# Kernel optimization log

Hardware: AMD Instinct MI355X
Metric: run time of the kernel (lower is better)

The kernel has to match this reference:

```python
import jax, jax.numpy as jnp
import numpy as np

IN_DIM = 256
QK_DIM = IN_DIM // 8  # 32
B, H, W = 4, 64, 64


def setup_inputs() -> dict:
    key = jax.random.key(0)
    ks = jax.random.split(key, 8)
    s = 1.0 / np.sqrt(IN_DIM)
    return {
        "x": jax.random.normal(ks[0], (B, IN_DIM, H, W), dtype=jnp.float32),
        "Wq": jax.random.normal(ks[1], (QK_DIM, IN_DIM), dtype=jnp.float32) * s,
        "bq": jax.random.normal(ks[2], (QK_DIM,), dtype=jnp.float32) * 0.01,
        "Wk": jax.random.normal(ks[3], (QK_DIM, IN_DIM), dtype=jnp.float32) * s,
        "bk": jax.random.normal(ks[4], (QK_DIM,), dtype=jnp.float32) * 0.01,
        "Wv": jax.random.normal(ks[5], (IN_DIM, IN_DIM), dtype=jnp.float32) * s,
        "bv": jax.random.normal(ks[6], (IN_DIM,), dtype=jnp.float32) * 0.01,
        "gamma": jax.random.normal(ks[7], (1,), dtype=jnp.float32) * 0.1,
    }


def reference(x, Wq, bq, Wk, bk, Wv, bv, gamma):
    b, c, h, w = x.shape
    n = h * w
    xf = x.reshape(b, c, n)  # [b, c, n]
    # 1x1 convs are channel-wise linear maps over flattened spatial dim
    q = jnp.einsum('dc,bcn->bnd', Wq, xf) + bq  # [b, n, d]
    k = jnp.einsum('dc,bcn->bdn', Wk, xf) + bk[:, None]  # [b, d, n]
    attn = jax.nn.softmax(jnp.einsum('bnd,bdm->bnm', q, k), axis=-1)  # [b, n, n]
    v = jnp.einsum('ec,bcn->ben', Wv, xf) + bv[:, None]  # [b, c, n]
    # out[:, :, m] = sum_n v[:, :, n] * attn[m, n]  (bmm with attn^T)
    out = jnp.einsum('ben,bmn->bem', v, attn).reshape(b, c, h, w)
    return gamma * out + x
```

## Files before the change

### kernel.cpp

```cpp
#include <hip/hip_runtime.h>
#include <hip/hip_bf16.h>
#include <stdint.h>

#define DI __device__ __forceinline__

typedef float f32x4 __attribute__((ext_vector_type(4)));
typedef short bf16x8 __attribute__((ext_vector_type(8)));

constexpr int BATCH = 4;
constexpr int C = 256;
constexpr int N = 4096;
constexpr int NO = 320;
constexpr int KB2 = 64;
constexpr int NT2 = N / KB2;
constexpr float LOG2E = 1.44269504088896340736f;

DI unsigned short f2bf(float f) {
  union { float f; unsigned int i; } v; v.f = f;
  unsigned int r = v.i + 0x7fffu + ((v.i >> 16) & 1u);
  return (unsigned short)(r >> 16);
}

DI float exp2i(float x) {
  float r; asm("v_exp_f32 %0, %1" : "=v"(r) : "v"(x)); return r;
}

DI unsigned int cvtpk(float lo, float hi) {
  unsigned int r;
  asm("v_cvt_pk_bf16_f32 %0, %1, %2" : "=v"(r) : "v"(lo), "v"(hi));
  return r;
}

__global__ __launch_bounds__(256) void prep_kernel(
    const float* __restrict__ Wq, const float* __restrict__ Wk, const float* __restrict__ Wv,
    const float* __restrict__ bq, const float* __restrict__ bk, const float* __restrict__ bv,
    unsigned short* __restrict__ Wcat, float* __restrict__ bcat) {
  int idx = blockIdx.x * 256 + threadIdx.x;
  if (idx < NO * C) {
    int row = idx >> 8, c = idx & 255;
    float v = (row < 32) ? Wq[row * 256 + c] * LOG2E
            : (row < 64) ? Wk[(row - 32) * 256 + c]
                         : Wv[(row - 64) * 256 + c];
    Wcat[idx] = f2bf(v);
  }
  if (idx < NO) {
    float v = (idx < 32) ? bq[idx] * LOG2E
            : (idx < 64) ? bk[idx - 32] : bv[idx - 64];
    bcat[idx] = v;
  }
}

__global__ __launch_bounds__(256) void proj_kernel(
    const float* __restrict__ x, const unsigned short* __restrict__ Wcat,
    const float* __restrict__ bcat,
    unsigned short* __restrict__ qarr, unsigned short* __restrict__ karr,
    unsigned short* __restrict__ vT) {
  __shared__ __align__(16) unsigned short ldsx[C][66];

  int b = blockIdx.y, n0 = blockIdx.x * 64, z = blockIdx.z;
  int t = threadIdx.x, lane = t & 63, w = t >> 6;
  int g = lane >> 4, cq = lane & 15;

  const float* xb = x + (size_t)b * C * N;
  {
    int csub = lane >> 4, m = lane & 15;
    #pragma unroll 4
    for (int cc = 0; cc < 16; ++cc) {
      int c = cc * 16 + w * 4 + csub;
      f32x4 v = *(const f32x4*)(xb + (size_t)c * N + n0 + m * 4);
      unsigned int p01 = ((unsigned int)f2bf(v[0])) | ((unsigned int)f2bf(v[1]) << 16);
      unsigned int p23 = ((unsigned int)f2bf(v[2])) | ((unsigned int)f2bf(v[3]) << 16);
      *(unsigned int*)(&ldsx[c][m * 4]) = p01;
      *(unsigned int*)(&ldsx[c][m * 4 + 2]) = p23;
    }
  }
  __syncthreads();

  bf16x8 afrag[8];
  int nrow = w * 16 + cq;
  #pragma unroll
  for (int ks = 0; ks < 8; ++ks) {
    bf16x8 a;
    #pragma unroll
    for (int j = 0; j < 8; ++j) a[j] = (short)ldsx[ks * 32 + g * 8 + j][nrow];
    afrag[ks] = a;
  }
  __syncthreads();

  unsigned short (*vlds)[66] = (unsigned short (*)[66]) & ldsx[0][0];

  #pragma unroll
  for (int i = 0; i < 4; ++i) {
    int oc = z * 4 + i;
    int o = oc * 16 + cq;
    f32x4 acc = {0.f, 0.f, 0.f, 0.f};
    const unsigned short* wrow = Wcat + o * 256;
    #pragma unroll
    for (int ks = 0; ks < 8; ++ks) {
      bf16x8 bf = *(const bf16x8*)(wrow + ks * 32 + g * 8);
      acc = __builtin_amdgcn_mfma_f32_16x16x32_bf16(afrag[ks], bf, acc, 0, 0, 0);
    }
    float bias = bcat[o];
    if (z == 0) {
      unsigned short* dst = (oc < 2) ? qarr : karr;
      int od = ((oc & 1) << 4) + cq;
      #pragma unroll
      for (int r = 0; r < 4; ++r) {
        int n = n0 + w * 16 + g * 4 + r;
        dst[((size_t)b * N + n) * 32 + od] = f2bf(acc[r] + bias);
      }
    } else {
      int el = i * 16 + cq;
      #pragma unroll
      for (int r = 0; r < 4; ++r)
        vlds[w * 16 + g * 4 + r][el] = f2bf(acc[r] + bias);
    }
  }

  if (z > 0) {
    __syncthreads();
    int e0 = (z - 1) * 64;
    #pragma unroll 4
    for (int ep = 0; ep < 16; ++ep) {
      int el = ep * 4 + w;
      vT[((size_t)b * 256 + e0 + el) * N + n0 + lane] = vlds[lane][el];
    }
  }
}

__global__ __launch_bounds__(512) void attn_kernel(
    const unsigned short* __restrict__ qarr, const unsigned short* __restrict__ karr,
    const unsigned short* __restrict__ vT, const float* __restrict__ x,
    const float* __restrict__ gamma_p, float* __restrict__ out) {
  __shared__ __align__(16) unsigned int plds[2][64][36];
  __shared__ float lsc[64];

  int bid = blockIdx.x;
  int xcd = bid & 7;
  int b = xcd >> 1;
  int eh = (bid >> 3) & 1;
  int tile = ((bid >> 4) << 1) | (bid & 1);

  int t = threadIdx.x, lane = t & 63, w = t >> 6;
  int g = lane >> 4, cq = lane & 15;
  int qw = w & 3, kh = w >> 2;

  const unsigned short* kb = karr + (size_t)b * N * 32;
  const unsigned short* vTb = vT + (size_t)b * C * N;

  bf16x8 qf = *(const bf16x8*)(qarr + ((size_t)b * N + tile * 64 + qw * 16 + cq) * 32 + g * 8);

  short onev = (cq == 0) ? (short)0x3F80 : (short)0;
  bf16x8 onesA = {onev, onev, onev, onev, onev, onev, onev, onev};

  f32x4 o[4];
  #pragma unroll
  for (int j = 0; j < 4; ++j) o[j] = f32x4{0.f, 0.f, 0.f, 0.f};
  f32x4 oL = {0.f, 0.f, 0.f, 0.f};

  const unsigned short* vbase = vTb + (size_t)(eh * 128 + w * 16 + cq) * N + g * 8;
  const unsigned short* kbase0 = kb + (size_t)(kh * 32 + 2 * cq) * 32 + g * 8;

  bf16x8 kf0 = *(const bf16x8*)(kbase0);
  bf16x8 kf1 = *(const bf16x8*)(kbase0 + 32);
  bf16x8 vf0 = *(const bf16x8*)(vbase);
  bf16x8 vf1 = *(const bf16x8*)(vbase + 32);

  const float C2 = 20.0f * LOG2E;

  for (int nt = 0; nt < NT2; ++nt) {
    int pb = nt & 1;
    int nn2 = ((nt + 1) & (NT2 - 1)) * KB2;

    bf16x8 nk0 = *(const bf16x8*)(kbase0 + (size_t)nn2 * 32);
    bf16x8 nk1 = *(const bf16x8*)(kbase0 + (size_t)nn2 * 32 + 32);
    bf16x8 nv0 = *(const bf16x8*)(vbase + nn2);
    bf16x8 nv1 = *(const bf16x8*)(vbase + nn2 + 32);

    f32x4 s0 = __builtin_amdgcn_mfma_f32_16x16x32_bf16(qf, kf0, f32x4{0.f,0.f,0.f,0.f}, 0, 0, 0);
    f32x4 s1 = __builtin_amdgcn_mfma_f32_16x16x32_bf16(qf, kf1, f32x4{0.f,0.f,0.f,0.f}, 0, 0, 0);

    #pragma unroll
    for (int r = 0; r < 4; ++r) {
      float p0 = exp2i(s0[r] - C2);
      float p1 = exp2i(s1[r] - C2);
      plds[pb][qw * 16 + g * 4 + r][kh * 16 + cq] = cvtpk(p0, p1);
    }

    asm volatile("s_waitcnt lgkmcnt(0)\n\ts_barrier" ::: "memory");

    __builtin_amdgcn_s_setprio(1);
    #pragma unroll
    for (int qc = 0; qc < 4; ++qc) {
      const unsigned short* prow = (const unsigned short*)&plds[pb][qc * 16 + cq][0];
      bf16x8 pf0 = *(const bf16x8*)(prow + g * 8);
      bf16x8 pf1 = *(const bf16x8*)(prow + 32 + g * 8);
      o[qc] = __builtin_amdgcn_mfma_f32_16x16x32_bf16(vf0, pf0, o[qc], 0, 0, 0);
      o[qc] = __builtin_amdgcn_mfma_f32_16x16x32_bf16(vf1, pf1, o[qc], 0, 0, 0);
      if (qc == w) {
        oL = __builtin_amdgcn_mfma_f32_16x16x32_bf16(onesA, pf0, oL, 0, 0, 0);
        oL = __builtin_amdgcn_mfma_f32_16x16x32_bf16(onesA, pf1, oL, 0, 0, 0);
      }
    }
    __builtin_amdgcn_s_setprio(0);

    kf0 = nk0; kf1 = nk1; vf0 = nv0; vf1 = nv1;
  }

  if (w < 4 && lane < 16) lsc[w * 16 + lane] = gamma_p[0] / oL[0];
  __syncthreads();

  const float* xb = x + (size_t)b * C * N;
  float* ob = out + (size_t)b * C * N;
  #pragma unroll
  for (int qc = 0; qc < 4; ++qc) {
    float scale = lsc[qc * 16 + cq];
    int qg = tile * 64 + qc * 16 + cq;
    #pragma unroll
    for (int r = 0; r < 4; ++r) {
      int e = eh * 128 + w * 16 + g * 4 + r;
      size_t idx = (size_t)e * N + qg;
      ob[idx] = o[qc][r] * scale + xb[idx];
    }
  }
}

extern "C" void kernel_launch(void* const* d_in, const int* in_sizes, int n_in,
                              void* d_out, int out_size, void* d_ws, size_t ws_size,
                              hipStream_t stream) {
  const float* x  = (const float*)d_in[0];
  const float* Wq = (const float*)d_in[1];
  const float* bq = (const float*)d_in[2];
  const float* Wk = (const float*)d_in[3];
  const float* bk = (const float*)d_in[4];
  const float* Wv = (const float*)d_in[5];
  const float* bv = (const float*)d_in[6];
  const float* gamma = (const float*)d_in[7];
  float* out = (float*)d_out;

  char* ws = (char*)d_ws;
  unsigned short* Wcat = (unsigned short*)(ws);
  float* bcat          = (float*)(ws + 163840);
  unsigned short* qarr = (unsigned short*)(ws + 165120);
  unsigned short* karr = (unsigned short*)(ws + 1213696);
  unsigned short* vT   = (unsigned short*)(ws + 2262272);

  prep_kernel<<<320, 256, 0, stream>>>(Wq, Wk, Wv, bq, bk, bv, Wcat, bcat);
  proj_kernel<<<dim3(64, 4, 5), 256, 0, stream>>>(x, Wcat, bcat, qarr, karr, vT);
  attn_kernel<<<512, 512, 0, stream>>>(qarr, karr, vT, x, gamma, out);
}
```

Measured before the change: 225.5 us.

## Retile attention to 32 queries by all channels and split projection grid finer

The attention kernel now gives each block 32 queries across all 256 output channels instead of 64 queries across half the channels. This removes the duplicated QK^T and exp work that the two channel-half blocks used to repeat, and it replaces the ones-matrix MFMA row-sum with per-lane fp32 accumulation followed by shuffle and LDS reduction. In exchange, each block streams the full V tile, which doubles total V reads from L2, and each wave holds more V fragments. Separately, the projection kernel's output split is doubled to 10 z-slices to increase parallelism, at the cost of reloading x into LDS more often.

New measurement: 241.0 us. 1.07x slower.

```diff
diff --git a/kernel.cpp b/kernel.cpp
--- a/kernel.cpp
+++ b/kernel.cpp
@@ -23,12 +23,6 @@
 
 DI float exp2i(float x) {
   float r; asm("v_exp_f32 %0, %1" : "=v"(r) : "v"(x)); return r;
-}
-
-DI unsigned int cvtpk(float lo, float hi) {
-  unsigned int r;
-  asm("v_cvt_pk_bf16_f32 %0, %1, %2" : "=v"(r) : "v"(lo), "v"(hi));
-  return r;
 }
 
 __global__ __launch_bounds__(256) void prep_kernel(
@@ -90,8 +84,8 @@
   unsigned short (*vlds)[66] = (unsigned short (*)[66]) & ldsx[0][0];
 
   #pragma unroll
-  for (int i = 0; i < 4; ++i) {
-    int oc = z * 4 + i;
+  for (int i = 0; i < 2; ++i) {
+    int oc = z * 2 + i;
     int o = oc * 16 + cq;
     f32x4 acc = {0.f, 0.f, 0.f, 0.f};
     const unsigned short* wrow = Wcat + o * 256;
@@ -101,8 +95,8 @@
       acc = __builtin_amdgcn_mfma_f32_16x16x32_bf16(afrag[ks], bf, acc, 0, 0, 0);
     }
     float bias = bcat[o];
-    if (z == 0) {
-      unsigned short* dst = (oc < 2) ? qarr : karr;
+    if (z < 2) {
+      unsigned short* dst = (z == 0) ? qarr : karr;
       int od = ((oc & 1) << 4) + cq;
       #pragma unroll
       for (int r = 0; r < 4; ++r) {
@@ -117,54 +111,56 @@
     }
   }
 
-  if (z > 0) {
+  if (z >= 2) {
     __syncthreads();
-    int e0 = (z - 1) * 64;
+    int e0 = (z - 2) * 32;
     #pragma unroll 4
-    for (int ep = 0; ep < 16; ++ep) {
+    for (int ep = 0; ep < 8; ++ep) {
       int el = ep * 4 + w;
       vT[((size_t)b * 256 + e0 + el) * N + n0 + lane] = vlds[lane][el];
     }
   }
 }
 
-__global__ __launch_bounds__(512) void attn_kernel(
+__global__ __launch_bounds__(512, 4) void attn_kernel(
     const unsigned short* __restrict__ qarr, const unsigned short* __restrict__ karr,
     const unsigned short* __restrict__ vT, const float* __restrict__ x,
     const float* __restrict__ gamma_p, float* __restrict__ out) {
-  __shared__ __align__(16) unsigned int plds[2][64][36];
-  __shared__ float lsc[64];
+  __shared__ __align__(16) unsigned short plds[2][32][136];
+  __shared__ float lred[4][32];
+  __shared__ float lsc[32];
 
   int bid = blockIdx.x;
   int xcd = bid & 7;
   int b = xcd >> 1;
-  int eh = (bid >> 3) & 1;
-  int tile = ((bid >> 4) << 1) | (bid & 1);
+  int tile = ((bid >> 3) << 1) | (bid & 1);
 
   int t = threadIdx.x, lane = t & 63, w = t >> 6;
   int g = lane >> 4, cq = lane & 15;
-  int qw = w & 3, kh = w >> 2;
+  int qw = w & 1, kh = w >> 1;
 
   const unsigned short* kb = karr + (size_t)b * N * 32;
   const unsigned short* vTb = vT + (size_t)b * C * N;
 
-  bf16x8 qf = *(const bf16x8*)(qarr + ((size_t)b * N + tile * 64 + qw * 16 + cq) * 32 + g * 8);
-
-  short onev = (cq == 0) ? (short)0x3F80 : (short)0;
-  bf16x8 onesA = {onev, onev, onev, onev, onev, onev, onev, onev};
-
-  f32x4 o[4];
-  #pragma unroll
-  for (int j = 0; j < 4; ++j) o[j] = f32x4{0.f, 0.f, 0.f, 0.f};
-  f32x4 oL = {0.f, 0.f, 0.f, 0.f};
-
-  const unsigned short* vbase = vTb + (size_t)(eh * 128 + w * 16 + cq) * N + g * 8;
-  const unsigned short* kbase0 = kb + (size_t)(kh * 32 + 2 * cq) * 32 + g * 8;
-
-  bf16x8 kf0 = *(const bf16x8*)(kbase0);
-  bf16x8 kf1 = *(const bf16x8*)(kbase0 + 32);
-  bf16x8 vf0 = *(const bf16x8*)(vbase);
-  bf16x8 vf1 = *(const bf16x8*)(vbase + 32);
+  bf16x8 qf = *(const bf16x8*)(qarr + ((size_t)b * N + tile * 32 + qw * 16 + cq) * 32 + g * 8);
+
+  f32x4 o[2][2];
+  #pragma unroll
+  for (int i = 0; i < 2; ++i)
+    #pragma unroll
+    for (int j = 0; j < 2; ++j) o[i][j] = f32x4{0.f, 0.f, 0.f, 0.f};
+  float Ls[4] = {0.f, 0.f, 0.f, 0.f};
+
+  const unsigned short* vbase = vTb + (size_t)(w * 32 + cq) * N + g * 8;
+  const unsigned short* kbase = kb + (size_t)(kh * 16 + cq) * 32 + g * 8;
+
+  bf16x8 kf = *(const bf16x8*)(kbase);
+  bf16x8 vf[2][2];
+  #pragma unroll
+  for (int ec = 0; ec < 2; ++ec)
+    #pragma unroll
+    for (int kc = 0; kc < 2; ++kc)
+      vf[ec][kc] = *(const bf16x8*)(vbase + (size_t)ec * 16 * N + kc * 32);
 
   const float C2 = 20.0f * LOG2E;
 
@@ -172,55 +168,76 @@
     int pb = nt & 1;
     int nn2 = ((nt + 1) & (NT2 - 1)) * KB2;
 
-    bf16x8 nk0 = *(const bf16x8*)(kbase0 + (size_t)nn2 * 32);
-    bf16x8 nk1 = *(const bf16x8*)(kbase0 + (size_t)nn2 * 32 + 32);
-    bf16x8 nv0 = *(const bf16x8*)(vbase + nn2);
-    bf16x8 nv1 = *(const bf16x8*)(vbase + nn2 + 32);
-
-    f32x4 s0 = __builtin_amdgcn_mfma_f32_16x16x32_bf16(qf, kf0, f32x4{0.f,0.f,0.f,0.f}, 0, 0, 0);
-    f32x4 s1 = __builtin_amdgcn_mfma_f32_16x16x32_bf16(qf, kf1, f32x4{0.f,0.f,0.f,0.f}, 0, 0, 0);
+    bf16x8 nk = *(const bf16x8*)(kbase + (size_t)nn2 * 32);
+    bf16x8 nv[2][2];
+    #pragma unroll
+    for (int ec = 0; ec < 2; ++ec)
+      #pragma unroll
+      for (int kc = 0; kc < 2; ++kc)
+        nv[ec][kc] = *(const bf16x8*)(vbase + (size_t)ec * 16 * N + nn2 + kc * 32);
+
+    f32x4 s = __builtin_amdgcn_mfma_f32_16x16x32_bf16(qf, kf, f32x4{0.f,0.f,0.f,0.f}, 0, 0, 0);
 
     #pragma unroll
     for (int r = 0; r < 4; ++r) {
-      float p0 = exp2i(s0[r] - C2);
-      float p1 = exp2i(s1[r] - C2);
-      plds[pb][qw * 16 + g * 4 + r][kh * 16 + cq] = cvtpk(p0, p1);
+      float p = exp2i(s[r] - C2);
+      Ls[r] += p;
+      plds[pb][qw * 16 + g * 4 + r][kh * 16 + cq] = f2bf(p);
     }
 
     asm volatile("s_waitcnt lgkmcnt(0)\n\ts_barrier" ::: "memory");
 
     __builtin_amdgcn_s_setprio(1);
     #pragma unroll
-    for (int qc = 0; qc < 4; ++qc) {
-      const unsigned short* prow = (const unsigned short*)&plds[pb][qc * 16 + cq][0];
+    for (int qc = 0; qc < 2; ++qc) {
+      const unsigned short* prow = &plds[pb][qc * 16 + cq][0];
       bf16x8 pf0 = *(const bf16x8*)(prow + g * 8);
       bf16x8 pf1 = *(const bf16x8*)(prow + 32 + g * 8);
-      o[qc] = __builtin_amdgcn_mfma_f32_16x16x32_bf16(vf0, pf0, o[qc], 0, 0, 0);
-      o[qc] = __builtin_amdgcn_mfma_f32_16x16x32_bf16(vf1, pf1, o[qc], 0, 0, 0);
-      if (qc == w) {
-        oL = __builtin_amdgcn_mfma_f32_16x16x32_bf16(onesA, pf0, oL, 0, 0, 0);
-        oL = __builtin_amdgcn_mfma_f32_16x16x32_bf16(onesA, pf1, oL, 0, 0, 0);
-      }
+      o[0][qc] = __builtin_amdgcn_mfma_f32_16x16x32_bf16(vf[0][0], pf0, o[0][qc], 0, 0, 0);
+      o[0][qc] = __builtin_amdgcn_mfma_f32_16x16x32_bf16(vf[0][1], pf1, o[0][qc], 0, 0, 0);
+      o[1][qc] = __builtin_amdgcn_mfma_f32_16x16x32_bf16(vf[1][0], pf0, o[1][qc], 0, 0, 0);
+      o[1][qc] = __builtin_amdgcn_mfma_f32_16x16x32_bf16(vf[1][1], pf1, o[1][qc], 0, 0, 0);
     }
     __builtin_amdgcn_s_setprio(0);
 
-    kf0 = nk0; kf1 = nk1; vf0 = nv0; vf1 = nv1;
-  }
-
-  if (w < 4 && lane < 16) lsc[w * 16 + lane] = gamma_p[0] / oL[0];
+    kf = nk;
+    #pragma unroll
+    for (int ec = 0; ec < 2; ++ec)
+      #pragma unroll
+      for (int kc = 0; kc < 2; ++kc)
+        vf[ec][kc] = nv[ec][kc];
+  }
+
+  #pragma unroll
+  for (int r = 0; r < 4; ++r) {
+    #pragma unroll
+    for (int d = 1; d <= 8; d <<= 1) Ls[r] += __shfl_xor(Ls[r], d);
+  }
+  if (cq == 0) {
+    #pragma unroll
+    for (int r = 0; r < 4; ++r) lred[kh][qw * 16 + g * 4 + r] = Ls[r];
+  }
+  __syncthreads();
+  if (t < 32) {
+    float L = lred[0][t] + lred[1][t] + lred[2][t] + lred[3][t];
+    lsc[t] = gamma_p[0] / L;
+  }
   __syncthreads();
 
   const float* xb = x + (size_t)b * C * N;
   float* ob = out + (size_t)b * C * N;
   #pragma unroll
-  for (int qc = 0; qc < 4; ++qc) {
+  for (int qc = 0; qc < 2; ++qc) {
     float scale = lsc[qc * 16 + cq];
-    int qg = tile * 64 + qc * 16 + cq;
-    #pragma unroll
-    for (int r = 0; r < 4; ++r) {
-      int e = eh * 128 + w * 16 + g * 4 + r;
-      size_t idx = (size_t)e * N + qg;
-      ob[idx] = o[qc][r] * scale + xb[idx];
+    int qg = tile * 32 + qc * 16 + cq;
+    #pragma unroll
+    for (int ec = 0; ec < 2; ++ec) {
+      #pragma unroll
+      for (int r = 0; r < 4; ++r) {
+        int e = w * 32 + ec * 16 + g * 4 + r;
+        size_t idx = (size_t)e * N + qg;
+        ob[idx] = o[ec][qc][r] * scale + xb[idx];
+      }
     }
   }
 }
@@ -246,6 +263,6 @@
   unsigned short* vT   = (unsigned short*)(ws + 2262272);
 
   prep_kernel<<<320, 256, 0, stream>>>(Wq, Wk, Wv, bq, bk, bv, Wcat, bcat);
-  proj_kernel<<<dim3(64, 4, 5), 256, 0, stream>>>(x, Wcat, bcat, qarr, karr, vT);
+  proj_kernel<<<dim3(64, 4, 10), 256, 0, stream>>>(x, Wcat, bcat, qarr, karr, vT);
   attn_kernel<<<512, 512, 0, stream>>>(qarr, karr, vT, x, gamma, out);
 }
```
